# Kernel tuning notes

Measured on AMD Instinct MI355X. Metric: run time of the kernel, lower is better.

Reference implementation:

```python
import jax, jax.numpy as jnp
import numpy as np

B = 65536
HID = 128
OUT = 10


def setup_inputs() -> dict:
    key = jax.random.key(0)
    ks = jax.random.split(key, 6)
    x = jax.random.normal(ks[0], (B, 784), dtype=jnp.float32)
    conv_w = jax.random.normal(ks[1], (3, 3), dtype=jnp.float32)
    # torch Linear(676,128): weight [128,676], bias [128]
    w1 = jax.random.normal(ks[2], (HID, 26 * 26), dtype=jnp.float32) * (1.0 / np.sqrt(26 * 26))
    b1 = jax.random.normal(ks[3], (HID,), dtype=jnp.float32) * 0.01
    w2 = jax.random.normal(ks[4], (OUT, HID), dtype=jnp.float32) * (1.0 / np.sqrt(HID))
    b2 = jax.random.normal(ks[5], (OUT,), dtype=jnp.float32) * 0.01
    return {"x": x, "conv_w": conv_w, "w1": w1, "b1": b1, "w2": w2, "b2": b2}


def reference(x, conv_w, w1, b1, w2, b2):
    b = x.shape[0]
    img = x.reshape(b, 1, 28, 28)                      # NCHW, single channel
    kern = conv_w.reshape(1, 1, 3, 3)                  # OIHW
    # valid 3x3 cross-correlation (matches the elementwise-multiply-and-sum loop)
    conv = jax.lax.conv_general_dilated(
        img, kern, window_strides=(1, 1), padding="VALID",
        dimension_numbers=("NCHW", "OIHW", "NCHW"))   # [B,1,26,26]
    feat = conv.reshape(b, 26 * 26)
    h = jax.nn.relu(feat @ w1.T + b1)                  # [B,128]
    return h @ w2.T + b2                               # [B,10]
```

## Files before the change

kernel.cpp:

```cpp
#include <hip/hip_runtime.h>
#include <hip/hip_bf16.h>

#define BATCH  65536
#define KREAL  784
#define BK     64
#define NCHUNK 13
#define HID    128
#define NOUT   10
#define BM     128
#define NTHR   512

using f32x4  = __attribute__((ext_vector_type(4))) float;
using short8 = __attribute__((ext_vector_type(8))) short;
using short4v= __attribute__((ext_vector_type(4))) short;
using f4     = __attribute__((ext_vector_type(4))) float;

__device__ inline short f2b(float f) {
    union { __hip_bfloat16 h; short s; } u;
    u.h = __float2bfloat16(f);
    return u.s;
}

#define GLDS16(gp, lp) \
    __builtin_amdgcn_global_load_lds((const __attribute__((address_space(1))) void*)(gp), \
                                     (__attribute__((address_space(3))) void*)(lp), 16, 0, 0)

#define NWB (NCHUNK*HID*BK)
#define NW2 (4*4*16*8)

__global__ void prep_kernel(const float* __restrict__ conv_w,
                            const float* __restrict__ w1,
                            const float* __restrict__ w2,
                            unsigned short* __restrict__ weff_sw,
                            unsigned short* __restrict__ w2f)
{
    int idx = blockIdx.x * 256 + threadIdx.x;
    if (idx < NWB) {
        int ic  = idx >> 13;
        int rem = idx & 8191;
        int r   = rem >> 6;
        int cc  = rem & 63;
        int g   = (cc >> 3) ^ (r & 7);
        int k   = ic * BK + g * 8 + (cc & 7);
        float acc = 0.f;
        if (k < KREAL) {
            int rr = k / 28, c = k - rr * 28;
            #pragma unroll
            for (int di = 0; di < 3; ++di) {
                int i = rr - di;
                if (i >= 0 && i < 26) {
                    #pragma unroll
                    for (int dj = 0; dj < 3; ++dj) {
                        int j = c - dj;
                        if (j >= 0 && j < 26)
                            acc = fmaf(w1[r * 676 + i * 26 + j], conv_w[di * 3 + dj], acc);
                    }
                }
            }
        }
        weff_sw[idx] = (unsigned short)f2b(acc);
    } else {
        int k2 = idx - NWB;
        if (k2 < NW2) {
            int e  = k2 & 7;
            int lo = (k2 >> 3) & 15;
            int hi = (k2 >> 7) & 3;
            int kk = k2 >> 9;
            float v = (lo < NOUT) ? w2[lo * HID + kk * 32 + hi * 8 + e] : 0.f;
            w2f[k2] = (unsigned short)f2b(v);
        }
    }
}

__global__ __launch_bounds__(NTHR, 4)
void fused_mlp_kernel(const float* __restrict__ x,
                      const float* __restrict__ b1,
                      const float* __restrict__ b2,
                      const unsigned short* __restrict__ weff_sw,
                      const unsigned short* __restrict__ w2f,
                      float* __restrict__ out)
{
    __shared__ __align__(16) unsigned char smem[65536];
    unsigned short* ldsA0 = (unsigned short*)smem;
    unsigned short* ldsA1 = (unsigned short*)(smem + 16384);
    unsigned short* ldsB0 = (unsigned short*)(smem + 32768);
    unsigned short* ldsB1 = (unsigned short*)(smem + 49152);
    unsigned short* ldsH  = (unsigned short*)smem;
    float*          outS  = (float*)(smem + 49152);

    const int tid  = threadIdx.x;
    const int wv   = tid >> 6;
    const int lane = tid & 63;
    const int lo   = lane & 15;
    const int hi   = lane >> 4;
    const int row0 = blockIdx.x * BM;
    const int wr0  = wv * 16;

    f32x4 acc[8];
    #pragma unroll
    for (int t = 0; t < 8; ++t) acc[t] = (f32x4){0.f, 0.f, 0.f, 0.f};

    const char* abase = (const char*)(x + (long)(row0 + wr0 + hi) * KREAL);
    f4 av[4];
    auto issueA = [&](int ic) {
        #pragma unroll
        for (int j = 0; j < 4; ++j) {
            int ce = ic * BK + lo * 4;
            int cb = (ce + 4 <= KREAL) ? ce : 0;
            av[j] = *(const f4*)(abase + (long)j * 4 * KREAL * 4 + (long)cb * 4);
        }
    };
    auto writeA = [&](unsigned short* dstA) {
        #pragma unroll
        for (int j = 0; j < 4; ++j) {
            int r = wr0 + j * 4 + hi;
            short4v c;
            c[0] = f2b(av[j][0]); c[1] = f2b(av[j][1]);
            c[2] = f2b(av[j][2]); c[3] = f2b(av[j][3]);
            int byteoff = r * 128 + ((((lo >> 1) ^ (r & 7)) << 4)) + ((lo & 1) << 3);
            *(short4v*)((char*)dstA + byteoff) = c;
        }
    };
    auto stageB = [&](int ic, unsigned short* dst) {
        const char* src = (const char*)(weff_sw + (long)ic * (HID * BK));
        GLDS16(src + wv * 2048 + lane * 16,        (char*)dst + wv * 2048);
        GLDS16(src + wv * 2048 + 1024 + lane * 16, (char*)dst + wv * 2048 + 1024);
    };

    issueA(0);
    stageB(0, ldsB0);
    asm volatile("s_waitcnt vmcnt(0)" ::: "memory");
    __builtin_amdgcn_sched_barrier(0);
    writeA(ldsA0);
    __builtin_amdgcn_s_barrier();
    __builtin_amdgcn_sched_barrier(0);

    #pragma unroll
    for (int ic = 0; ic < NCHUNK; ++ic) {
        const unsigned short* Ac = (ic & 1) ? ldsA1 : ldsA0;
        const unsigned short* Bc = (ic & 1) ? ldsB1 : ldsB0;
        if (ic + 1 < NCHUNK) {
            issueA(ic + 1);
            stageB(ic + 1, (ic & 1) ? ldsB0 : ldsB1);
        }
        const int r = wr0 + lo;
        #pragma unroll
        for (int kk = 0; kk < 2; ++kk) {
            const int G = kk * 4 + hi;
            short8 af = *(const short8*)((const char*)Ac + r * 128 + ((G ^ (r & 7)) << 4));
            #pragma unroll
            for (int t = 0; t < 8; ++t) {
                const int ob = t * 16 + lo;
                short8 bfrag = *(const short8*)&Bc[ob * BK + ((G ^ (ob & 7)) << 3)];
                acc[t] = __builtin_amdgcn_mfma_f32_16x16x32_bf16(af, bfrag, acc[t], 0, 0, 0);
            }
        }
        if (ic + 1 < NCHUNK) {
            __builtin_amdgcn_sched_barrier(0);
            asm volatile("s_waitcnt vmcnt(0)" ::: "memory");
            __builtin_amdgcn_sched_barrier(0);
            writeA((ic & 1) ? ldsA0 : ldsA1);
            __builtin_amdgcn_sched_barrier(0);
            __builtin_amdgcn_s_barrier();
            __builtin_amdgcn_sched_barrier(0);
        }
    }

    __builtin_amdgcn_sched_barrier(0);
    __builtin_amdgcn_s_barrier();
    __builtin_amdgcn_sched_barrier(0);

    #pragma unroll
    for (int t = 0; t < 8; ++t) {
        float bias = b1[t * 16 + lo];
        #pragma unroll
        for (int j = 0; j < 4; ++j) {
            float hv = acc[t][j] + bias;
            hv = hv > 0.f ? hv : 0.f;
            int rloc = wr0 + hi * 4 + j;
            int col  = t * 16 + lo;
            int g    = col >> 3, e = col & 7;
            ldsH[rloc * HID + ((g ^ (rloc & 7)) << 3) + e] = (unsigned short)f2b(hv);
        }
    }

    f32x4 acc2 = (f32x4){0.f, 0.f, 0.f, 0.f};
    #pragma unroll
    for (int kk = 0; kk < 4; ++kk) {
        int r = wr0 + lo;
        int g = kk * 4 + hi;
        short8 ha = *(const short8*)&ldsH[r * HID + ((g ^ (r & 7)) << 3)];
        short8 wb = *(const short8*)(w2f + (((kk * 4 + hi) * 16 + lo) << 3));
        acc2 = __builtin_amdgcn_mfma_f32_16x16x32_bf16(ha, wb, acc2, 0, 0, 0);
    }
    float* os = outS + wv * 160;
    if (lo < NOUT) {
        float bb = b2[lo];
        #pragma unroll
        for (int j = 0; j < 4; ++j)
            os[(hi * 4 + j) * NOUT + lo] = acc2[j] + bb;
    }
    if (lane < 40) {
        f4 v = *(const f4*)&os[lane * 4];
        *(f4*)(out + (long)(row0 + wr0) * NOUT + lane * 4) = v;
    }
}

extern "C" void kernel_launch(void* const* d_in, const int* in_sizes, int n_in,
                              void* d_out, int out_size, void* d_ws, size_t ws_size,
                              hipStream_t stream)
{
    const float* x      = (const float*)d_in[0];
    const float* conv_w = (const float*)d_in[1];
    const float* w1     = (const float*)d_in[2];
    const float* b1     = (const float*)d_in[3];
    const float* w2     = (const float*)d_in[4];
    const float* b2     = (const float*)d_in[5];
    float* out = (float*)d_out;

    unsigned short* weff_sw = (unsigned short*)d_ws;
    unsigned short* w2f     = weff_sw + NWB;

    const int prep_total = NWB + NW2;
    prep_kernel<<<(prep_total + 255) / 256, 256, 0, stream>>>(conv_w, w1, w2, weff_sw, w2f);
    fused_mlp_kernel<<<BATCH / BM, NTHR, 0, stream>>>(x, b1, b2, weff_sw, w2f, out);
}
```

Baseline: 43.67 us.

## Stage activation tile in 256-column superchunks with deeper prefetch and split vmcnt waits

The activation tile now loads in 256-column superchunks: each wave fetches 16 rows × 256 fp32 columns into registers and writes them as bf16 into a single 64KB swizzled LDS buffer once every four K-chunks. The weight chunks stay double-buffered in LDS, and the vmcnt waits are split so the A prefetch stays in flight over two chunks. The aim is fewer, larger global loads of x and fewer per-chunk A conversions and LDS writes, which should hide more of the HBM latency. In exchange, dynamic LDS grows to 96KB and launch bounds are relaxed, which likely cuts resident blocks per CU and adds register pressure.

After: 53.23 us. 1.22x slower.

```diff
diff --git a/kernel.cpp b/kernel.cpp
--- a/kernel.cpp
+++ b/kernel.cpp
@@ -72,7 +72,7 @@
     }
 }
 
-__global__ __launch_bounds__(NTHR, 4)
+__global__ __launch_bounds__(NTHR, 2)
 void fused_mlp_kernel(const float* __restrict__ x,
                       const float* __restrict__ b1,
                       const float* __restrict__ b2,
@@ -80,13 +80,12 @@
                       const unsigned short* __restrict__ w2f,
                       float* __restrict__ out)
 {
-    __shared__ __align__(16) unsigned char smem[65536];
-    unsigned short* ldsA0 = (unsigned short*)smem;
-    unsigned short* ldsA1 = (unsigned short*)(smem + 16384);
-    unsigned short* ldsB0 = (unsigned short*)(smem + 32768);
-    unsigned short* ldsB1 = (unsigned short*)(smem + 49152);
+    extern __shared__ __align__(16) unsigned char smem[];
+    unsigned short* ldsA  = (unsigned short*)smem;
+    unsigned short* ldsB0 = (unsigned short*)(smem + 65536);
+    unsigned short* ldsB1 = (unsigned short*)(smem + 81920);
     unsigned short* ldsH  = (unsigned short*)smem;
-    float*          outS  = (float*)(smem + 49152);
+    float*          outS  = (float*)(smem + 65536);
 
     const int tid  = threadIdx.x;
     const int wv   = tid >> 6;
@@ -100,25 +99,25 @@
     #pragma unroll
     for (int t = 0; t < 8; ++t) acc[t] = (f32x4){0.f, 0.f, 0.f, 0.f};
 
-    const char* abase = (const char*)(x + (long)(row0 + wr0 + hi) * KREAL);
-    f4 av[4];
-    auto issueA = [&](int ic) {
-        #pragma unroll
-        for (int j = 0; j < 4; ++j) {
-            int ce = ic * BK + lo * 4;
+    f4 av[16];
+    const char* abase = (const char*)x + (long)(row0 + wr0) * (KREAL * 4);
+    auto issueA = [&](int sc) {
+        #pragma unroll
+        for (int j = 0; j < 16; ++j) {
+            int ce = sc * 256 + lane * 4;
             int cb = (ce + 4 <= KREAL) ? ce : 0;
-            av[j] = *(const f4*)(abase + (long)j * 4 * KREAL * 4 + (long)cb * 4);
+            av[j] = *(const f4*)(abase + (long)j * (KREAL * 4) + (long)cb * 4);
         }
     };
-    auto writeA = [&](unsigned short* dstA) {
-        #pragma unroll
-        for (int j = 0; j < 4; ++j) {
-            int r = wr0 + j * 4 + hi;
+    auto writeA = [&]() {
+        #pragma unroll
+        for (int j = 0; j < 16; ++j) {
+            int r = wr0 + j;
             short4v c;
             c[0] = f2b(av[j][0]); c[1] = f2b(av[j][1]);
             c[2] = f2b(av[j][2]); c[3] = f2b(av[j][3]);
-            int byteoff = r * 128 + ((((lo >> 1) ^ (r & 7)) << 4)) + ((lo & 1) << 3);
-            *(short4v*)((char*)dstA + byteoff) = c;
+            int byteoff = r * 512 + ((((lane >> 1) ^ (r & 15)) << 4)) + ((lane & 1) << 3);
+            *(short4v*)((char*)ldsA + byteoff) = c;
         }
     };
     auto stageB = [&](int ic, unsigned short* dst) {
@@ -127,39 +126,52 @@
         GLDS16(src + wv * 2048 + 1024 + lane * 16, (char*)dst + wv * 2048 + 1024);
     };
 
+    stageB(0, ldsB0);
     issueA(0);
-    stageB(0, ldsB0);
     asm volatile("s_waitcnt vmcnt(0)" ::: "memory");
     __builtin_amdgcn_sched_barrier(0);
-    writeA(ldsA0);
+    writeA();
     __builtin_amdgcn_s_barrier();
     __builtin_amdgcn_sched_barrier(0);
 
     #pragma unroll
-    for (int ic = 0; ic < NCHUNK; ++ic) {
-        const unsigned short* Ac = (ic & 1) ? ldsA1 : ldsA0;
-        const unsigned short* Bc = (ic & 1) ? ldsB1 : ldsB0;
-        if (ic + 1 < NCHUNK) {
-            issueA(ic + 1);
-            stageB(ic + 1, (ic & 1) ? ldsB0 : ldsB1);
-        }
+    for (int c = 0; c < NCHUNK; ++c) {
+        const int sc = c >> 2;
+        const int u  = c & 3;
+        const unsigned short* Bc = (c & 1) ? ldsB1 : ldsB0;
+
+        if (c + 1 < NCHUNK)
+            stageB(c + 1, (c & 1) ? ldsB0 : ldsB1);
+        if (u == 2 && sc < 3)
+            issueA(sc + 1);
+
         const int r = wr0 + lo;
         #pragma unroll
         for (int kk = 0; kk < 2; ++kk) {
-            const int G = kk * 4 + hi;
-            short8 af = *(const short8*)((const char*)Ac + r * 128 + ((G ^ (r & 7)) << 4));
+            const int GA = u * 8 + kk * 4 + hi;
+            short8 af = *(const short8*)((const char*)ldsA + r * 512 + ((GA ^ (r & 15)) << 4));
+            const int GB = kk * 4 + hi;
             #pragma unroll
             for (int t = 0; t < 8; ++t) {
                 const int ob = t * 16 + lo;
-                short8 bfrag = *(const short8*)&Bc[ob * BK + ((G ^ (ob & 7)) << 3)];
+                short8 bfrag = *(const short8*)&Bc[ob * BK + ((GB ^ (ob & 7)) << 3)];
                 acc[t] = __builtin_amdgcn_mfma_f32_16x16x32_bf16(af, bfrag, acc[t], 0, 0, 0);
             }
         }
-        if (ic + 1 < NCHUNK) {
+
+        if (c + 1 < NCHUNK) {
             __builtin_amdgcn_sched_barrier(0);
-            asm volatile("s_waitcnt vmcnt(0)" ::: "memory");
-            __builtin_amdgcn_sched_barrier(0);
-            writeA((ic & 1) ? ldsA0 : ldsA1);
+            if (u == 3) {
+                asm volatile("s_waitcnt vmcnt(2)" ::: "memory");
+                __builtin_amdgcn_sched_barrier(0);
+                writeA();
+                __builtin_amdgcn_sched_barrier(0);
+                asm volatile("s_waitcnt vmcnt(0)" ::: "memory");
+            } else if (u == 2) {
+                asm volatile("s_waitcnt vmcnt(16)" ::: "memory");
+            } else {
+                asm volatile("s_waitcnt vmcnt(0)" ::: "memory");
+            }
             __builtin_amdgcn_sched_barrier(0);
             __builtin_amdgcn_s_barrier();
             __builtin_amdgcn_sched_barrier(0);
@@ -223,5 +235,5 @@
 
     const int prep_total = NWB + NW2;
     prep_kernel<<<(prep_total + 255) / 256, 256, 0, stream>>>(conv_w, w1, w2, weff_sw, w2f);
-    fused_mlp_kernel<<<BATCH / BM, NTHR, 0, stream>>>(x, b1, b2, weff_sw, w2f, out);
-}
+    fused_mlp_kernel<<<BATCH / BM, NTHR, 98304, stream>>>(x, b1, b2, weff_sw, w2f, out);
+}
```

## Halve block tile, single-buffer per-wave A tile, and rotate K-chunk start per block

Applied to the files above, without the earlier changes.

Cuts the block to 64 rows with 256 threads. Each block gets a smaller LDS footprint (one A tile instead of two) and there are twice as many blocks, so more blocks can fit per CU and the grid balances better across CUs. Each block now starts its K loop at a chunk offset based on block index, so concurrent blocks read different parts of the folded weight matrix instead of all hitting the same chunk. The A tile is single-buffered, which is safe only because each wave reads and writes only its own rows. The A conversion store now happens before the explicit wait, which gives less overlap per block.

Result: no change. 43.29 us (median of 2 runs) (-0.9%).

```diff
diff --git a/kernel.cpp b/kernel.cpp
--- a/kernel.cpp
+++ b/kernel.cpp
@@ -7,8 +7,8 @@
 #define NCHUNK 13
 #define HID    128
 #define NOUT   10
-#define BM     128
-#define NTHR   512
+#define BM     64
+#define NTHR   256
 
 using f32x4  = __attribute__((ext_vector_type(4))) float;
 using short8 = __attribute__((ext_vector_type(8))) short;
@@ -80,13 +80,12 @@
                       const unsigned short* __restrict__ w2f,
                       float* __restrict__ out)
 {
-    __shared__ __align__(16) unsigned char smem[65536];
-    unsigned short* ldsA0 = (unsigned short*)smem;
-    unsigned short* ldsA1 = (unsigned short*)(smem + 16384);
-    unsigned short* ldsB0 = (unsigned short*)(smem + 32768);
-    unsigned short* ldsB1 = (unsigned short*)(smem + 49152);
+    __shared__ __align__(16) unsigned char smem[40960];
+    unsigned short* ldsA  = (unsigned short*)smem;
+    unsigned short* ldsB0 = (unsigned short*)(smem + 8192);
+    unsigned short* ldsB1 = (unsigned short*)(smem + 24576);
     unsigned short* ldsH  = (unsigned short*)smem;
-    float*          outS  = (float*)(smem + 49152);
+    float*          outS  = (float*)(smem + 16384);
 
     const int tid  = threadIdx.x;
     const int wv   = tid >> 6;
@@ -95,6 +94,7 @@
     const int hi   = lane >> 4;
     const int row0 = blockIdx.x * BM;
     const int wr0  = wv * 16;
+    const int c0   = blockIdx.x % NCHUNK;
 
     f32x4 acc[8];
     #pragma unroll
@@ -110,7 +110,7 @@
             av[j] = *(const f4*)(abase + (long)j * 4 * KREAL * 4 + (long)cb * 4);
         }
     };
-    auto writeA = [&](unsigned short* dstA) {
+    auto writeA = [&]() {
         #pragma unroll
         for (int j = 0; j < 4; ++j) {
             int r = wr0 + j * 4 + hi;
@@ -118,36 +118,39 @@
             c[0] = f2b(av[j][0]); c[1] = f2b(av[j][1]);
             c[2] = f2b(av[j][2]); c[3] = f2b(av[j][3]);
             int byteoff = r * 128 + ((((lo >> 1) ^ (r & 7)) << 4)) + ((lo & 1) << 3);
-            *(short4v*)((char*)dstA + byteoff) = c;
+            *(short4v*)((char*)ldsA + byteoff) = c;
         }
     };
     auto stageB = [&](int ic, unsigned short* dst) {
         const char* src = (const char*)(weff_sw + (long)ic * (HID * BK));
-        GLDS16(src + wv * 2048 + lane * 16,        (char*)dst + wv * 2048);
-        GLDS16(src + wv * 2048 + 1024 + lane * 16, (char*)dst + wv * 2048 + 1024);
+        #pragma unroll
+        for (int j = 0; j < 4; ++j)
+            GLDS16(src + wv * 4096 + j * 1024 + lane * 16,
+                   (char*)dst + wv * 4096 + j * 1024);
     };
 
-    issueA(0);
-    stageB(0, ldsB0);
+    issueA(c0);
+    stageB(c0, ldsB0);
+    writeA();
     asm volatile("s_waitcnt vmcnt(0)" ::: "memory");
     __builtin_amdgcn_sched_barrier(0);
-    writeA(ldsA0);
     __builtin_amdgcn_s_barrier();
     __builtin_amdgcn_sched_barrier(0);
 
     #pragma unroll
-    for (int ic = 0; ic < NCHUNK; ++ic) {
-        const unsigned short* Ac = (ic & 1) ? ldsA1 : ldsA0;
-        const unsigned short* Bc = (ic & 1) ? ldsB1 : ldsB0;
-        if (ic + 1 < NCHUNK) {
-            issueA(ic + 1);
-            stageB(ic + 1, (ic & 1) ? ldsB0 : ldsB1);
+    for (int s = 0; s < NCHUNK; ++s) {
+        int ic  = c0 + s;     if (ic >= NCHUNK)  ic -= NCHUNK;
+        int icn = ic + 1;     if (icn >= NCHUNK) icn -= NCHUNK;
+        const unsigned short* Bc = (s & 1) ? ldsB1 : ldsB0;
+        if (s + 1 < NCHUNK) {
+            issueA(icn);
+            stageB(icn, (s & 1) ? ldsB0 : ldsB1);
         }
         const int r = wr0 + lo;
         #pragma unroll
         for (int kk = 0; kk < 2; ++kk) {
             const int G = kk * 4 + hi;
-            short8 af = *(const short8*)((const char*)Ac + r * 128 + ((G ^ (r & 7)) << 4));
+            short8 af = *(const short8*)((const char*)ldsA + r * 128 + ((G ^ (r & 7)) << 4));
             #pragma unroll
             for (int t = 0; t < 8; ++t) {
                 const int ob = t * 16 + lo;
@@ -155,11 +158,11 @@
                 acc[t] = __builtin_amdgcn_mfma_f32_16x16x32_bf16(af, bfrag, acc[t], 0, 0, 0);
             }
         }
-        if (ic + 1 < NCHUNK) {
+        if (s + 1 < NCHUNK) {
+            __builtin_amdgcn_sched_barrier(0);
+            writeA();
             __builtin_amdgcn_sched_barrier(0);
             asm volatile("s_waitcnt vmcnt(0)" ::: "memory");
-            __builtin_amdgcn_sched_barrier(0);
-            writeA((ic & 1) ? ldsA0 : ldsA1);
             __builtin_amdgcn_sched_barrier(0);
             __builtin_amdgcn_s_barrier();
             __builtin_amdgcn_sched_barrier(0);
```
